# Performance work log

Hardware: AMD Instinct MI355X
Metric: run time of the kernel (lower is better)

## Reference

```python
import jax, jax.numpy as jnp
import numpy as np

EDGE_TEXT_IMG = 2
D_MODEL = 256
N_HEADS = 8
N_LAYERS = 3
INPUT_DIM = 768
LN_EPS = 1e-5
CONFLICT_EPS = 1e-6


def setup_inputs() -> dict:
    key = jax.random.key(0)
    ks = jax.random.split(key, 32)
    B, N, E = 16, 512, 4096
    d, H, L = D_MODEL, N_HEADS, N_LAYERS
    s = 0.02
    inp = {
        'node_feats': jax.random.normal(ks[0], (B, N, INPUT_DIM), jnp.float32),
        'node_mask': jnp.ones((B, N), bool),
        'text_mask': jax.random.randint(ks[1], (B, N), 0, 2).astype(bool),
        'image_mask': jax.random.randint(ks[2], (B, N), 0, 2).astype(bool),
        'global_indices': jax.random.randint(ks[3], (B,), 0, N),
        'edge_index': jax.random.randint(ks[4], (B, 2, E), 0, N),
        'edge_type': jax.random.randint(ks[5], (B, E), 0, 4),
        'edge_weight': jax.random.uniform(ks[6], (B, E), jnp.float32),
        # params
        'W_in': jax.random.normal(ks[7], (INPUT_DIM, d)) * s,
        'b_in': jnp.zeros((d,)),
        'Wqkv': jax.random.normal(ks[8], (L, d, 3 * d)) * s,
        'bqkv': jnp.zeros((L, 3 * d)),
        'Wo': jax.random.normal(ks[9], (L, d, d)) * s,
        'bo': jnp.zeros((L, d)),
        'ln1_g': jnp.ones((L, d)), 'ln1_b': jnp.zeros((L, d)),
        'ln2_g': jnp.ones((L, d)), 'ln2_b': jnp.zeros((L, d)),
        'Wff1': jax.random.normal(ks[10], (L, d, 4 * d)) * s,
        'bff1': jnp.zeros((L, 4 * d)),
        'Wff2': jax.random.normal(ks[11], (L, 4 * d, d)) * s,
        'bff2': jnp.zeros((L, d)),
        'et_emb': jax.random.normal(ks[12], (4, H)) * s,
        'Wm1': jax.random.normal(ks[13], (3 * d + 1, 2 * d)) * s,
        'bm1': jnp.zeros((2 * d,)),
        'Wm2': jax.random.normal(ks[14], (2 * d, d)) * s,
        'bm2': jnp.zeros((d,)),
        'Wm3': jax.random.normal(ks[15], (d, 1)) * s,
        'bm3': jnp.zeros((1,)),
    }
    return inp


def _ln(x, g, b):
    mu = jnp.mean(x, -1, keepdims=True)
    var = jnp.mean((x - mu) ** 2, -1, keepdims=True)
    return (x - mu) * jax.lax.rsqrt(var + LN_EPS) * g + b


def _build_bias(edge_index, edge_type, edge_weight, et_emb, N):
    # vectorized scatter-add of per-edge head biases into dense [B,H,N,N]
    B = edge_index.shape[0]
    src, dst = edge_index[:, 0], edge_index[:, 1]  # [B,E]
    vals = et_emb[edge_type]  # [B,E,H]
    vals = vals + jnp.where(edge_type == EDGE_TEXT_IMG, edge_weight, 0.0)[..., None]
    bias = jnp.zeros((B, N, N, et_emb.shape[1]), vals.dtype)
    bias = bias.at[jnp.arange(B)[:, None], src, dst].add(vals)
    return bias.transpose(0, 3, 1, 2)  # [B,H,N,N]


def _forward(node_feats, node_mask, text_mask, image_mask, global_indices,
             edge_index, edge_type, edge_weight,
             W_in, b_in, Wqkv, bqkv, Wo, bo, ln1_g, ln1_b, ln2_g, ln2_b,
             Wff1, bff1, Wff2, bff2, et_emb, Wm1, bm1, Wm2, bm2, Wm3, bm3):
    B, N, _ = node_feats.shape
    H = N_HEADS
    hd = D_MODEL // H
    attn_bias = _build_bias(edge_index, edge_type, edge_weight, et_emb, N)
    x = node_feats @ W_in + b_in  # [B,N,d]
    key_mask = node_mask[:, None, None, :]  # [B,1,1,N]
    for l in range(N_LAYERS):
        qkv = x @ Wqkv[l] + bqkv[l]
        qkv = qkv.reshape(B, N, 3, H, hd).transpose(2, 0, 3, 1, 4)
        q, k, v = qkv[0], qkv[1], qkv[2]  # [B,H,N,hd]
        scores = jnp.einsum('bhnd,bhmd->bhnm', q, k) / np.sqrt(hd).astype(np.float32)
        scores = scores + attn_bias
        scores = jnp.where(key_mask, scores, -jnp.inf)
        attn = jax.nn.softmax(scores, axis=-1)
        out = jnp.einsum('bhnm,bhmd->bhnd', attn, v)
        out = out.transpose(0, 2, 1, 3).reshape(B, N, D_MODEL)
        out = out @ Wo[l] + bo[l]
        x = _ln(x + out, ln1_g[l], ln1_b[l])
        ff = jax.nn.gelu(x @ Wff1[l] + bff1[l], approximate=False) @ Wff2[l] + bff2[l]
        x = _ln(x + ff, ln2_g[l], ln2_b[l])
    tm = text_mask.astype(x.dtype)
    im = image_mask.astype(x.dtype)
    tc = jnp.clip(tm.sum(1, keepdims=True), 1.0)
    ic = jnp.clip(im.sum(1, keepdims=True), 1.0)
    text_pool = (x * tm[..., None]).sum(1) / tc
    image_pool = (x * im[..., None]).sum(1) / ic
    global_embeds = x[jnp.arange(B), global_indices]
    n1 = jnp.maximum(jnp.linalg.norm(text_pool, axis=-1), CONFLICT_EPS)
    n2 = jnp.maximum(jnp.linalg.norm(image_pool, axis=-1), CONFLICT_EPS)
    cos = jnp.sum(text_pool * image_pool, -1) / (n1 * n2)
    conflict = (1.0 - cos)[:, None]
    combined = jnp.concatenate([global_embeds, text_pool, image_pool, conflict], -1)
    h = jax.nn.gelu(combined @ Wm1 + bm1, approximate=False)
    h = jax.nn.gelu(h @ Wm2 + bm2, approximate=False)
    logits = (h @ Wm3 + bm3)[:, 0]
    return logits


def reference(node_feats, node_mask, text_mask, image_mask, global_indices,
              edge_index, edge_type, edge_weight,
              W_in, b_in, Wqkv, bqkv, Wo, bo, ln1_g, ln1_b, ln2_g, ln2_b,
              Wff1, bff1, Wff2, bff2, et_emb, Wm1, bm1, Wm2, bm2, Wm3, bm3):
    return _forward(node_feats, node_mask, text_mask, image_mask, global_indices,
                    edge_index, edge_type, edge_weight,
                    W_in, b_in, Wqkv, bqkv, Wo, bo, ln1_g, ln1_b, ln2_g, ln2_b,
                    Wff1, bff1, Wff2, bff2, et_emb, Wm1, bm1, Wm2, bm2, Wm3, bm3)
```

## Files before the change

### kernel.cpp

```cpp
#include <hip/hip_runtime.h>
#include <hip/hip_bf16.h>
#include <math.h>

#define Bb 16
#define Nn 512
#define Dd 256
#define Hh 8
#define HD 32
#define Ll 3
#define INDIM 768
#define Ee 4096
#define FF 1024
#define KP3 36
#define KP2 72
#define NBUCK 32768

typedef unsigned short u16;
typedef __bf16 bf16x8 __attribute__((ext_vector_type(8)));
typedef float f32x4 __attribute__((ext_vector_type(4)));
typedef u16 us8 __attribute__((ext_vector_type(8)));
typedef u16 us4 __attribute__((ext_vector_type(4)));

__device__ __forceinline__ float gelu_exact(float x) {
    return 0.5f * x * (1.0f + erff(x * 0.70710678118654752f));
}

__device__ __forceinline__ u16 f2bf(float x) {
    union { __bf16 b; u16 u; } cv;
    cv.b = (__bf16)x;
    return cv.u;
}
__device__ __forceinline__ float bf2f(u16 h) {
    return __uint_as_float(((unsigned int)h) << 16);
}

__device__ __forceinline__ int ebucket(int b, int src, int dst) {
    return ((b * 32 + (src >> 4)) * 4 + (dst >> 7)) * 16 + (src & 15);
}

__device__ __forceinline__ int xcd_swz(int bid, int nwg) {
    int chunk = nwg >> 3;
    return (bid & 7) * chunk + (bid >> 3);
}


__global__ __launch_bounds__(256) void zero2_kernel(int* __restrict__ a, int na,
                                                    int* __restrict__ b, int nb) {
    int gid = blockIdx.x * 256 + threadIdx.x;
    if (gid < na) a[gid] = 0;
    else {
        int j = gid - na;
        if (j < nb) b[j] = 0;
    }
}

__global__ __launch_bounds__(256) void count_kernel(const int* __restrict__ edge_index,
                                                    int* __restrict__ counts) {
    int gid = blockIdx.x * 256 + threadIdx.x;
    int b = gid >> 12;
    int e = gid & (Ee - 1);
    int src = edge_index[b * 2 * Ee + e];
    int dst = edge_index[b * 2 * Ee + Ee + e];
    atomicAdd(&counts[ebucket(b, src, dst)], 1);
}

__global__ __launch_bounds__(1024) void scan_kernel(const int* __restrict__ counts,
                                                    int* __restrict__ offsets,
                                                    int* __restrict__ cursor) {
    __shared__ int ssum[1024];
    int t = threadIdx.x;
    int local[32];
    int s = 0;
#pragma unroll
    for (int i = 0; i < 32; i++) { local[i] = counts[t * 32 + i]; s += local[i]; }
    ssum[t] = s;
    __syncthreads();
    for (int off = 1; off < 1024; off *= 2) {
        __syncthreads();
        int v = (t >= off) ? ssum[t - off] : 0;
        __syncthreads();
        ssum[t] += v;
    }
    __syncthreads();
    int base = (t > 0) ? ssum[t - 1] : 0;
#pragma unroll
    for (int i = 0; i < 32; i++) {
        offsets[t * 32 + i] = base;
        cursor[t * 32 + i] = base;
        base += local[i];
    }
    if (t == 1023) offsets[NBUCK] = base;
}

__global__ __launch_bounds__(256) void scatter_kernel(const int* __restrict__ edge_index,
                                                      const int* __restrict__ edge_type,
                                                      const float* __restrict__ edge_weight,
                                                      int* __restrict__ cursor,
                                                      int2* __restrict__ pelist) {
    int gid = blockIdx.x * 256 + threadIdx.x;
    int b = gid >> 12;
    int e = gid & (Ee - 1);
    int src = edge_index[b * 2 * Ee + e];
    int dst = edge_index[b * 2 * Ee + Ee + e];
    int ty = edge_type[b * Ee + e];
    float wgt = edge_weight[b * Ee + e];
    int pos = atomicAdd(&cursor[ebucket(b, src, dst)], 1);
    int2 pe;
    pe.x = (src << 20) | (dst << 4) | ty;
    pe.y = __float_as_int(wgt);
    pelist[pos] = pe;
}


#define OFF_IN  0
#define OFF_QKV 196608
#define OFF_O   786432
#define OFF_F1  983040
#define OFF_F2  1769472
#define W_TOTAL 2555904

__global__ __launch_bounds__(256) void wsplit_all(const float* __restrict__ W_in,
                                                  const float* __restrict__ Wqkv,
                                                  const float* __restrict__ Wo,
                                                  const float* __restrict__ Wff1,
                                                  const float* __restrict__ Wff2,
                                                  u16* __restrict__ wh,
                                                  u16* __restrict__ wl) {
    int bid = blockIdx.x;
    const float* W;
    u16 *Wh, *Wl;
    int K, N, nb, kb;
    if (bid < 96) {
        W = W_in; Wh = wh + OFF_IN; Wl = wl + OFF_IN;
        K = 768; N = 256; nb = 0; kb = bid;
    } else if (bid < 384) {
        int lb = bid - 96; int l = lb / 96; lb -= l * 96;
        W = Wqkv + (size_t)l * 196608;
        Wh = wh + OFF_QKV + (size_t)l * 196608;
        Wl = wl + OFF_QKV + (size_t)l * 196608;
        K = 256; N = 768; nb = lb % 3; kb = lb / 3;
    } else if (bid < 480) {
        int lb = bid - 384; int l = lb / 32; lb -= l * 32;
        W = Wo + (size_t)l * 65536;
        Wh = wh + OFF_O + (size_t)l * 65536;
        Wl = wl + OFF_O + (size_t)l * 65536;
        K = 256; N = 256; nb = 0; kb = lb;
    } else if (bid < 864) {
        int lb = bid - 480; int l = lb / 128; lb -= l * 128;
        W = Wff1 + (size_t)l * 262144;
        Wh = wh + OFF_F1 + (size_t)l * 262144;
        Wl = wl + OFF_F1 + (size_t)l * 262144;
        K = 256; N = 1024; nb = lb % 4; kb = lb / 4;
    } else {
        int lb = bid - 864; int l = lb / 128; lb -= l * 128;
        W = Wff2 + (size_t)l * 262144;
        Wh = wh + OFF_F2 + (size_t)l * 262144;
        Wl = wl + OFF_F2 + (size_t)l * 262144;
        K = 1024; N = 256; nb = 0; kb = lb;
    }
    int n = nb * 256 + threadIdx.x;
    int k0 = kb * 8;
    float w[8];
#pragma unroll
    for (int i = 0; i < 8; i++) w[i] = W[(size_t)(k0 + i) * N + n];
    u16 h[8], l[8];
#pragma unroll
    for (int i = 0; i < 8; i++) {
        h[i] = f2bf(w[i]);
        l[i] = f2bf(w[i] - bf2f(h[i]));
    }
    us8 hv = {h[0], h[1], h[2], h[3], h[4], h[5], h[6], h[7]};
    us8 lv = {l[0], l[1], l[2], l[3], l[4], l[5], l[6], l[7]};
    *(us8*)&Wh[(size_t)n * K + k0] = hv;
    *(us8*)&Wl[(size_t)n * K + k0] = lv;
}


__global__ __launch_bounds__(256, 2) void gemm_mfma64(const float* __restrict__ A,
                                                      const u16* __restrict__ Bh,
                                                      const u16* __restrict__ Bl,
                                                      const float* __restrict__ bias,
                                                      float* __restrict__ C,
                                                      int M, int K, int N, int act) {
    __shared__ u16 sAh[2][64 * KP2];
    __shared__ u16 sAl[2][64 * KP2];
    __shared__ u16 sBh[2][64 * KP2];
    __shared__ u16 sBl[2][64 * KP2];

    int t = threadIdx.x;
    int w = t >> 6, L = t & 63;
    int wr = w >> 1, wc = w & 1;
    int lane15 = L & 15, quad = L >> 4;
    int nbx = N >> 6;
    int orig = xcd_swz(blockIdx.x, gridDim.x);
    int by = orig / nbx;
    int bx = orig - by * nbx;
    int row0 = by * 64, col0 = bx * 64;

    f32x4 acc[2][2];
#pragma unroll
    for (int mi = 0; mi < 2; mi++)
#pragma unroll
        for (int ni = 0; ni < 2; ni++) acc[mi][ni] = {0.f, 0.f, 0.f, 0.f};

    int ar0 = t >> 3, ak0 = (t & 7) * 8;
    int bn0 = t >> 2, bk0 = (t & 3) * 16;

    const float* Ap0 = &A[(size_t)(row0 + ar0) * K + ak0];
    const float* Ap1 = &A[(size_t)(row0 + ar0 + 32) * K + ak0];
    const u16* Bhp = &Bh[(size_t)(col0 + bn0) * K + bk0];
    const u16* Blp = &Bl[(size_t)(col0 + bn0) * K + bk0];

    float4 av0[2], av1[2];
    us8 bhv[2], blv[2];
#pragma unroll
    for (int j = 0; j < 2; j++) {
        av0[j] = *(const float4*)&Ap0[4 * j];
        av1[j] = *(const float4*)&Ap1[4 * j];
        bhv[j] = *(const us8*)&Bhp[8 * j];
        blv[j] = *(const us8*)&Blp[8 * j];
    }

    int nit = K >> 6;

#pragma unroll
    for (int j = 0; j < 2; j++) {
        {
            float a[4] = {av0[j].x, av0[j].y, av0[j].z, av0[j].w};
            u16 h[4], l[4];
#pragma unroll
            for (int q = 0; q < 4; q++) { h[q] = f2bf(a[q]); l[q] = f2bf(a[q] - bf2f(h[q])); }
            us4 hv = {h[0], h[1], h[2], h[3]};
            us4 lv = {l[0], l[1], l[2], l[3]};
            *(us4*)&sAh[0][ar0 * KP2 + ak0 + 4 * j] = hv;
            *(us4*)&sAl[0][ar0 * KP2 + ak0 + 4 * j] = lv;
        }
        {
            float a[4] = {av1[j].x, av1[j].y, av1[j].z, av1[j].w};
            u16 h[4], l[4];
#pragma unroll
            for (int q = 0; q < 4; q++) { h[q] = f2bf(a[q]); l[q] = f2bf(a[q] - bf2f(h[q])); }
            us4 hv = {h[0], h[1], h[2], h[3]};
            us4 lv = {l[0], l[1], l[2], l[3]};
            *(us4*)&sAh[0][(ar0 + 32) * KP2 + ak0 + 4 * j] = hv;
            *(us4*)&sAl[0][(ar0 + 32) * KP2 + ak0 + 4 * j] = lv;
        }
        *(us8*)&sBh[0][bn0 * KP2 + bk0 + 8 * j] = bhv[j];
        *(us8*)&sBl[0][bn0 * KP2 + bk0 + 8 * j] = blv[j];
    }
    if (nit > 1) {
#pragma unroll
        for (int j = 0; j < 2; j++) {
            av0[j] = *(const float4*)&Ap0[64 + 4 * j];
            av1[j] = *(const float4*)&Ap1[64 + 4 * j];
            bhv[j] = *(const us8*)&Bhp[64 + 8 * j];
            blv[j] = *(const us8*)&Blp[64 + 8 * j];
        }
    }

    for (int i = 0; i < nit; i++) {
        __syncthreads();
        int cur = i & 1;
        if (i + 1 < nit) {
            int nxt = cur ^ 1;
#pragma unroll
            for (int j = 0; j < 2; j++) {
                {
                    float a[4] = {av0[j].x, av0[j].y, av0[j].z, av0[j].w};
                    u16 h[4], l[4];
#pragma unroll
                    for (int q = 0; q < 4; q++) { h[q] = f2bf(a[q]); l[q] = f2bf(a[q] - bf2f(h[q])); }
                    us4 hv = {h[0], h[1], h[2], h[3]};
                    us4 lv = {l[0], l[1], l[2], l[3]};
                    *(us4*)&sAh[nxt][ar0 * KP2 + ak0 + 4 * j] = hv;
                    *(us4*)&sAl[nxt][ar0 * KP2 + ak0 + 4 * j] = lv;
                }
                {
                    float a[4] = {av1[j].x, av1[j].y, av1[j].z, av1[j].w};
                    u16 h[4], l[4];
#pragma unroll
                    for (int q = 0; q < 4; q++) { h[q] = f2bf(a[q]); l[q] = f2bf(a[q] - bf2f(h[q])); }
                    us4 hv = {h[0], h[1], h[2], h[3]};
                    us4 lv = {l[0], l[1], l[2], l[3]};
                    *(us4*)&sAh[nxt][(ar0 + 32) * KP2 + ak0 + 4 * j] = hv;
                    *(us4*)&sAl[nxt][(ar0 + 32) * KP2 + ak0 + 4 * j] = lv;
                }
                *(us8*)&sBh[nxt][bn0 * KP2 + bk0 + 8 * j] = bhv[j];
                *(us8*)&sBl[nxt][bn0 * KP2 + bk0 + 8 * j] = blv[j];
            }
            if (i + 2 < nit) {
                int ko = (i + 2) * 64;
#pragma unroll
                for (int j = 0; j < 2; j++) {
                    av0[j] = *(const float4*)&Ap0[ko + 4 * j];
                    av1[j] = *(const float4*)&Ap1[ko + 4 * j];
                    bhv[j] = *(const us8*)&Bhp[ko + 8 * j];
                    blv[j] = *(const us8*)&Blp[ko + 8 * j];
                }
            }
        }

#pragma unroll
        for (int half = 0; half < 2; half++) {
            int kof = half * 32 + quad * 8;
            us8 ahr[2], alr[2], bhr[2], blr[2];
#pragma unroll
            for (int mi = 0; mi < 2; mi++) {
                int ro = (wr * 32 + mi * 16 + lane15) * KP2 + kof;
                ahr[mi] = *(const us8*)&sAh[cur][ro];
                alr[mi] = *(const us8*)&sAl[cur][ro];
            }
#pragma unroll
            for (int ni = 0; ni < 2; ni++) {
                int ro = (wc * 32 + ni * 16 + lane15) * KP2 + kof;
                bhr[ni] = *(const us8*)&sBh[cur][ro];
                blr[ni] = *(const us8*)&sBl[cur][ro];
            }
#pragma unroll
            for (int mi = 0; mi < 2; mi++) {
                bf16x8 ah = *(const bf16x8*)&ahr[mi];
                bf16x8 al = *(const bf16x8*)&alr[mi];
#pragma unroll
                for (int ni = 0; ni < 2; ni++) {
                    bf16x8 bh = *(const bf16x8*)&bhr[ni];
                    bf16x8 bl = *(const bf16x8*)&blr[ni];
                    acc[mi][ni] = __builtin_amdgcn_mfma_f32_16x16x32_bf16(ah, bh, acc[mi][ni], 0, 0, 0);
                    acc[mi][ni] = __builtin_amdgcn_mfma_f32_16x16x32_bf16(ah, bl, acc[mi][ni], 0, 0, 0);
                    acc[mi][ni] = __builtin_amdgcn_mfma_f32_16x16x32_bf16(al, bh, acc[mi][ni], 0, 0, 0);
                }
            }
        }
    }

#pragma unroll
    for (int mi = 0; mi < 2; mi++) {
#pragma unroll
        for (int ni = 0; ni < 2; ni++) {
            int col = col0 + wc * 32 + ni * 16 + lane15;
            float bcol = bias[col];
#pragma unroll
            for (int r = 0; r < 4; r++) {
                int row = row0 + wr * 32 + mi * 16 + quad * 4 + r;
                float u = acc[mi][ni][r] + bcol;
                if (act == 1) u = gelu_exact(u);
                C[(size_t)row * N + col] = u;
            }
        }
    }
}


__global__ __launch_bounds__(512, 2) void gemm_mfma128(const float* __restrict__ A,
                                                       const u16* __restrict__ Bh,
                                                       const u16* __restrict__ Bl,
                                                       const float* __restrict__ bias,
                                                       float* __restrict__ C,
                                                       int M, int K, int N, int act) {
    __shared__ u16 sAh[2][128 * KP3];
    __shared__ u16 sAl[2][128 * KP3];
    __shared__ u16 sBh[2][128 * KP3];
    __shared__ u16 sBl[2][128 * KP3];

    int t = threadIdx.x;
    int w = t >> 6, L = t & 63;
    int wr = w >> 2, wc = w & 3;
    int lane15 = L & 15, quad = L >> 4;
    int nbx = N >> 7;
    int orig = xcd_swz(blockIdx.x, gridDim.x);
    int by = orig / nbx;
    int bx = orig - by * nbx;
    int row0 = by * 128, col0 = bx * 128;

    f32x4 acc[4][2];
#pragma unroll
    for (int mi = 0; mi < 4; mi++)
#pragma unroll
        for (int ni = 0; ni < 2; ni++) acc[mi][ni] = {0.f, 0.f, 0.f, 0.f};

    int ar0 = t >> 2, ak0 = (t & 3) * 8;
    int bn0 = t >> 2, bk0 = (t & 3) * 8;

    const float* Ap = &A[(size_t)(row0 + ar0) * K + ak0];
    const u16* Bhp = &Bh[(size_t)(col0 + bn0) * K + bk0];
    const u16* Blp = &Bl[(size_t)(col0 + bn0) * K + bk0];

    float4 av[2];
    us8 bhv, blv;
    av[0] = *(const float4*)&Ap[0];
    av[1] = *(const float4*)&Ap[4];
    bhv = *(const us8*)&Bhp[0];
    blv = *(const us8*)&Blp[0];

    int nit = K >> 5;

    {
        float a[8] = {av[0].x, av[0].y, av[0].z, av[0].w, av[1].x, av[1].y, av[1].z, av[1].w};
        u16 h[8], l[8];
#pragma unroll
        for (int q = 0; q < 8; q++) { h[q] = f2bf(a[q]); l[q] = f2bf(a[q] - bf2f(h[q])); }
        us8 hv = {h[0], h[1], h[2], h[3], h[4], h[5], h[6], h[7]};
        us8 lv = {l[0], l[1], l[2], l[3], l[4], l[5], l[6], l[7]};
        *(us8*)&sAh[0][ar0 * KP3 + ak0] = hv;
        *(us8*)&sAl[0][ar0 * KP3 + ak0] = lv;
        *(us8*)&sBh[0][bn0 * KP3 + bk0] = bhv;
        *(us8*)&sBl[0][bn0 * KP3 + bk0] = blv;
    }
    if (nit > 1) {
        av[0] = *(const float4*)&Ap[32];
        av[1] = *(const float4*)&Ap[36];
        bhv = *(const us8*)&Bhp[32];
        blv = *(const us8*)&Blp[32];
    }

    for (int it = 0; it < nit; it++) {
        __syncthreads();
        int cur = it & 1;
        if (it + 1 < nit) {
            int nxt = cur ^ 1;
            float a[8] = {av[0].x, av[0].y, av[0].z, av[0].w, av[1].x, av[1].y, av[1].z, av[1].w};
            u16 h[8], l[8];
#pragma unroll
            for (int q = 0; q < 8; q++) { h[q] = f2bf(a[q]); l[q] = f2bf(a[q] - bf2f(h[q])); }
            us8 hv = {h[0], h[1], h[2], h[3], h[4], h[5], h[6], h[7]};
            us8 lv = {l[0], l[1], l[2], l[3], l[4], l[5], l[6], l[7]};
            *(us8*)&sAh[nxt][ar0 * KP3 + ak0] = hv;
            *(us8*)&sAl[nxt][ar0 * KP3 + ak0] = lv;
            *(us8*)&sBh[nxt][bn0 * KP3 + bk0] = bhv;
            *(us8*)&sBl[nxt][bn0 * KP3 + bk0] = blv;
            if (it + 2 < nit) {
                int ko = (it + 2) * 32;
                av[0] = *(const float4*)&Ap[ko];
                av[1] = *(const float4*)&Ap[ko + 4];
                bhv = *(const us8*)&Bhp[ko];
                blv = *(const us8*)&Blp[ko];
            }
        }

        int kof = quad * 8;
        us8 ahr[4], alr[4], bhr[2], blr[2];
#pragma unroll
        for (int mi = 0; mi < 4; mi++) {
            int ro = (wr * 64 + mi * 16 + lane15) * KP3 + kof;
            ahr[mi] = *(const us8*)&sAh[cur][ro];
            alr[mi] = *(const us8*)&sAl[cur][ro];
        }
#pragma unroll
        for (int ni = 0; ni < 2; ni++) {
            int ro = (wc * 32 + ni * 16 + lane15) * KP3 + kof;
            bhr[ni] = *(const us8*)&sBh[cur][ro];
            blr[ni] = *(const us8*)&sBl[cur][ro];
        }
#pragma unroll
        for (int mi = 0; mi < 4; mi++) {
            bf16x8 ah = *(const bf16x8*)&ahr[mi];
            bf16x8 al = *(const bf16x8*)&alr[mi];
#pragma unroll
            for (int ni = 0; ni < 2; ni++) {
                bf16x8 bh = *(const bf16x8*)&bhr[ni];
                bf16x8 bl = *(const bf16x8*)&blr[ni];
                acc[mi][ni] = __builtin_amdgcn_mfma_f32_16x16x32_bf16(ah, bh, acc[mi][ni], 0, 0, 0);
                acc[mi][ni] = __builtin_amdgcn_mfma_f32_16x16x32_bf16(ah, bl, acc[mi][ni], 0, 0, 0);
                acc[mi][ni] = __builtin_amdgcn_mfma_f32_16x16x32_bf16(al, bh, acc[mi][ni], 0, 0, 0);
            }
        }
    }

#pragma unroll
    for (int mi = 0; mi < 4; mi++) {
#pragma unroll
        for (int ni = 0; ni < 2; ni++) {
            int col = col0 + wc * 32 + ni * 16 + lane15;
            float bcol = bias[col];
#pragma unroll
            for (int r = 0; r < 4; r++) {
                int row = row0 + wr * 64 + mi * 16 + quad * 4 + r;
                float u = acc[mi][ni][r] + bcol;
                if (act == 1) u = gelu_exact(u);
                C[(size_t)row * N + col] = u;
            }
        }
    }
}


#define SBP 132

__global__ __launch_bounds__(256, 2) void attn_kernel(const float* __restrict__ qkv,
                                                      const int* __restrict__ node_mask,
                                                      const int* __restrict__ offsets,
                                                      const int2* __restrict__ pelist,
                                                      const float* __restrict__ et_emb,
                                                      float* __restrict__ outbuf) {
    int bid = xcd_swz(blockIdx.x, gridDim.x);
    int quarter = bid & 3;
    int h = (bid >> 2) & 7;
    int b = bid >> 5;
    int t = threadIdx.x;
    int w = t >> 6, L = t & 63;
    int quad = L >> 4, lane15 = L & 15;
    int q8 = quad * 8;

    __shared__ u16 sKh[128 * 40];
    __shared__ u16 sKl[128 * 40];
    __shared__ u16 sVh[32 * SBP];
    __shared__ u16 sVl[32 * SBP];
    __shared__ float sS[4 * 16 * SBP];

    float* Sw = &sS[w * 16 * SBP];
    const float scale = 0.17677669529663687f;
    int nbase = quarter * 128 + w * 32;
    int mt0 = t >> 5, dt = t & 31;

    float etl0 = et_emb[0 * Hh + h];
    float etl1 = et_emb[1 * Hh + h];
    float etl2 = et_emb[2 * Hh + h];
    float etl3 = et_emb[3 * Hh + h];

    us8 Qh[2], Ql[2];
#pragma unroll
    for (int sub = 0; sub < 2; sub++) {
        size_t row = (size_t)(b * Nn + nbase + sub * 16 + lane15);
        float4 qa = *(const float4*)&qkv[row * 768 + h * HD + q8];
        float4 qb = *(const float4*)&qkv[row * 768 + h * HD + q8 + 4];
        float qv[8] = {qa.x, qa.y, qa.z, qa.w, qb.x, qb.y, qb.z, qb.w};
#pragma unroll
        for (int j = 0; j < 8; j++) {
            float xq = qv[j] * scale;
            u16 hh = f2bf(xq);
            Qh[sub][j] = hh;
            Ql[sub][j] = f2bf(xq - bf2f(hh));
        }
    }

    float Mst[2] = {-INFINITY, -INFINITY};
    float Lst[2] = {0.0f, 0.0f};
    f32x4 O[2][2];
#pragma unroll
    for (int sub = 0; sub < 2; sub++)
#pragma unroll
        for (int dc = 0; dc < 2; dc++) O[sub][dc] = {0.f, 0.f, 0.f, 0.f};

    float pk[16], pv[16];
#pragma unroll
    for (int j = 0; j < 16; j++) {
        size_t grow = (size_t)(b * Nn + mt0 + 8 * j) * 768 + h * HD + dt;
        pk[j] = qkv[grow + 256];
        pv[j] = qkv[grow + 512];
    }

    for (int T = 0; T < 4; T++) {
        int m0 = T * 128;
        __syncthreads();
#pragma unroll
        for (int j = 0; j < 16; j++) {
            int m = mt0 + 8 * j;
            u16 kh = f2bf(pk[j]);
            sKh[m * 40 + dt] = kh;
            sKl[m * 40 + dt] = f2bf(pk[j] - bf2f(kh));
            u16 vh = f2bf(pv[j]);
            sVh[dt * SBP + m] = vh;
            sVl[dt * SBP + m] = f2bf(pv[j] - bf2f(vh));
        }
        __syncthreads();
        if (T < 3) {
#pragma unroll
            for (int j = 0; j < 16; j++) {
                size_t grow = (size_t)(b * Nn + (T + 1) * 128 + mt0 + 8 * j) * 768 + h * HD + dt;
                pk[j] = qkv[grow + 256];
                pv[j] = qkv[grow + 512];
            }
        }

        float mk[4][8];
#pragma unroll
        for (int c = 0; c < 4; c++) {
            int4 u0 = *(const int4*)&node_mask[b * Nn + m0 + c * 32 + q8];
            int4 u1 = *(const int4*)&node_mask[b * Nn + m0 + c * 32 + q8 + 4];
            mk[c][0] = u0.x ? 0.f : -INFINITY;
            mk[c][1] = u0.y ? 0.f : -INFINITY;
            mk[c][2] = u0.z ? 0.f : -INFINITY;
            mk[c][3] = u0.w ? 0.f : -INFINITY;
            mk[c][4] = u1.x ? 0.f : -INFINITY;
            mk[c][5] = u1.y ? 0.f : -INFINITY;
            mk[c][6] = u1.z ? 0.f : -INFINITY;
            mk[c][7] = u1.w ? 0.f : -INFINITY;
        }

#pragma unroll
        for (int sub = 0; sub < 2; sub++) {
            int nsub = nbase + sub * 16;
            bf16x8 qh = *(const bf16x8*)&Qh[sub];
            bf16x8 ql = *(const bf16x8*)&Ql[sub];

            f32x4 accS[8];
#pragma unroll
            for (int mc = 0; mc < 8; mc++) accS[mc] = {0.f, 0.f, 0.f, 0.f};
#pragma unroll
            for (int mc = 0; mc < 8; mc++) {
                us8 khr = *(const us8*)&sKh[(mc * 16 + lane15) * 40 + q8];
                us8 klr = *(const us8*)&sKl[(mc * 16 + lane15) * 40 + q8];
                bf16x8 kh = *(const bf16x8*)&khr;
                bf16x8 kl = *(const bf16x8*)&klr;
                accS[mc] = __builtin_amdgcn_mfma_f32_16x16x32_bf16(qh, kh, accS[mc], 0, 0, 0);
                accS[mc] = __builtin_amdgcn_mfma_f32_16x16x32_bf16(qh, kl, accS[mc], 0, 0, 0);
                accS[mc] = __builtin_amdgcn_mfma_f32_16x16x32_bf16(ql, kh, accS[mc], 0, 0, 0);
            }
#pragma unroll
            for (int mc = 0; mc < 8; mc++)
#pragma unroll
                for (int r = 0; r < 4; r++)
                    Sw[(quad * 4 + r) * SBP + mc * 16 + lane15] = accS[mc][r];
            asm volatile("s_waitcnt lgkmcnt(0)" ::: "memory");

            int gb = ((b * 32 + (nsub >> 4)) * 4 + T) * 16;
            int beg = offsets[gb];
            int end = offsets[gb + 16];
            for (int i = beg + L; i < end; i += 64) {
                int2 pe = pelist[i];
                int sx = pe.x >> 20;
                int dx = (pe.x >> 4) & 511;
                int ty = pe.x & 3;
                float wgt = __int_as_float(pe.y);
                float val = (ty == 0) ? etl0 : (ty == 1) ? etl1 : (ty == 2) ? etl2 : etl3;
                if (ty == 2) val += wgt;
                atomicAdd(&Sw[(sx - nsub) * SBP + (dx - m0)], val);
            }
            asm volatile("s_waitcnt lgkmcnt(0)" ::: "memory");

            float s[4][8];
#pragma unroll
            for (int c = 0; c < 4; c++) {
                float4 a = *(const float4*)&Sw[lane15 * SBP + c * 32 + q8];
                float4 bq = *(const float4*)&Sw[lane15 * SBP + c * 32 + q8 + 4];
                s[c][0] = a.x + mk[c][0];  s[c][1] = a.y + mk[c][1];
                s[c][2] = a.z + mk[c][2];  s[c][3] = a.w + mk[c][3];
                s[c][4] = bq.x + mk[c][4]; s[c][5] = bq.y + mk[c][5];
                s[c][6] = bq.z + mk[c][6]; s[c][7] = bq.w + mk[c][7];
            }
            float mx = s[0][0];
#pragma unroll
            for (int c = 0; c < 4; c++)
#pragma unroll
                for (int j = 0; j < 8; j++) mx = fmaxf(mx, s[c][j]);
            mx = fmaxf(mx, __shfl_xor(mx, 16));
            mx = fmaxf(mx, __shfl_xor(mx, 32));
            float Mnew = fmaxf(Mst[sub], mx);
            float alpha = __expf(Mst[sub] - Mnew);
            float rs = 0.0f;
#pragma unroll
            for (int c = 0; c < 4; c++)
#pragma unroll
                for (int j = 0; j < 8; j++) {
                    s[c][j] = __expf(s[c][j] - Mnew);
                    rs += s[c][j];
                }
            rs += __shfl_xor(rs, 16);
            rs += __shfl_xor(rs, 32);
            Lst[sub] = Lst[sub] * alpha + rs;
            Mst[sub] = Mnew;

            us8 Ph[4], Pl[4];
#pragma unroll
            for (int c = 0; c < 4; c++)
#pragma unroll
                for (int j = 0; j < 8; j++) {
                    u16 ph = f2bf(s[c][j]);
                    Ph[c][j] = ph;
                    Pl[c][j] = f2bf(s[c][j] - bf2f(ph));
                }

            float aD[4];
#pragma unroll
            for (int r = 0; r < 4; r++) aD[r] = __shfl(alpha, (L & 48) | (quad * 4 + r));
#pragma unroll
            for (int dc = 0; dc < 2; dc++)
#pragma unroll
                for (int r = 0; r < 4; r++) O[sub][dc][r] *= aD[r];

#pragma unroll
            for (int c = 0; c < 4; c++) {
                bf16x8 ph = *(const bf16x8*)&Ph[c];
                bf16x8 pl = *(const bf16x8*)&Pl[c];
#pragma unroll
                for (int dc = 0; dc < 2; dc++) {
                    us8 vhr = *(const us8*)&sVh[(dc * 16 + lane15) * SBP + c * 32 + q8];
                    us8 vlr = *(const us8*)&sVl[(dc * 16 + lane15) * SBP + c * 32 + q8];
                    bf16x8 vh = *(const bf16x8*)&vhr;
                    bf16x8 vl = *(const bf16x8*)&vlr;
                    O[sub][dc] = __builtin_amdgcn_mfma_f32_16x16x32_bf16(ph, vh, O[sub][dc], 0, 0, 0);
                    O[sub][dc] = __builtin_amdgcn_mfma_f32_16x16x32_bf16(ph, vl, O[sub][dc], 0, 0, 0);
                    O[sub][dc] = __builtin_amdgcn_mfma_f32_16x16x32_bf16(pl, vh, O[sub][dc], 0, 0, 0);
                }
            }
        }
    }

#pragma unroll
    for (int sub = 0; sub < 2; sub++) {
        float linv = 1.0f / Lst[sub];
        float lD[4];
#pragma unroll
        for (int r = 0; r < 4; r++) lD[r] = __shfl(linv, (L & 48) | (quad * 4 + r));
#pragma unroll
        for (int dc = 0; dc < 2; dc++)
#pragma unroll
            for (int r = 0; r < 4; r++) {
                int row = nbase + sub * 16 + quad * 4 + r;
                outbuf[(size_t)(b * Nn + row) * Dd + h * HD + dc * 16 + lane15] =
                    O[sub][dc][r] * lD[r];
            }
    }
}


__global__ __launch_bounds__(256) void ln_kernel(float* __restrict__ x,
                                                 const float* __restrict__ res,
                                                 const float* __restrict__ g,
                                                 const float* __restrict__ bta) {
    int row = blockIdx.x * 4 + (threadIdx.x >> 6);
    int L = threadIdx.x & 63;
    size_t base = (size_t)row * Dd + L * 4;
    float4 v4 = *(const float4*)&x[base];
    float4 r4 = *(const float4*)&res[base];
    float v0 = v4.x + r4.x, v1 = v4.y + r4.y, v2 = v4.z + r4.z, v3 = v4.w + r4.w;
    float sm = v0 + v1 + v2 + v3;
#pragma unroll
    for (int o = 32; o > 0; o >>= 1) sm += __shfl_xor(sm, o);
    float mu = sm * (1.0f / Dd);
    float d0 = v0 - mu, d1 = v1 - mu, d2 = v2 - mu, d3 = v3 - mu;
    float s2 = d0 * d0 + d1 * d1 + d2 * d2 + d3 * d3;
#pragma unroll
    for (int o = 32; o > 0; o >>= 1) s2 += __shfl_xor(s2, o);
    float rsig = 1.0f / sqrtf(s2 * (1.0f / Dd) + 1e-5f);
    float4 g4 = *(const float4*)&g[L * 4];
    float4 b4 = *(const float4*)&bta[L * 4];
    float4 o4;
    o4.x = d0 * rsig * g4.x + b4.x;
    o4.y = d1 * rsig * g4.y + b4.y;
    o4.z = d2 * rsig * g4.z + b4.z;
    o4.w = d3 * rsig * g4.w + b4.w;
    *(float4*)&x[base] = o4;
}


__global__ __launch_bounds__(256) void pool_kernel(const float* __restrict__ x,
                                                   const int* __restrict__ text_mask,
                                                   const int* __restrict__ image_mask,
                                                   float* __restrict__ pools) {
    int b = blockIdx.y;
    int n0 = blockIdx.x * 32;
    int t = threadIdx.x;
    float tp = 0.0f, ip = 0.0f, c1 = 0.0f, c2 = 0.0f;
    for (int n = n0; n < n0 + 32; n++) {
        float xv = x[(size_t)(b * Nn + n) * Dd + t];
        int tm = text_mask[b * Nn + n];
        int im = image_mask[b * Nn + n];
        tp += tm ? xv : 0.0f;
        ip += im ? xv : 0.0f;
        c1 += (float)tm;
        c2 += (float)im;
    }
    atomicAdd(&pools[b * 514 + t], tp);
    atomicAdd(&pools[b * 514 + 256 + t], ip);
    if (t == 0) {
        atomicAdd(&pools[b * 514 + 512], c1);
        atomicAdd(&pools[b * 514 + 513], c2);
    }
}

__global__ __launch_bounds__(256) void comb_kernel(const float* __restrict__ x,
                                                   const float* __restrict__ pools,
                                                   const int* __restrict__ gidx,
                                                   float* __restrict__ comb) {
    int b = blockIdx.x;
    int t = threadIdx.x;
    __shared__ float redd[12];
    float tc = fmaxf(pools[b * 514 + 512], 1.0f);
    float ic = fmaxf(pools[b * 514 + 513], 1.0f);
    float tp = pools[b * 514 + t] / tc;
    float ip = pools[b * 514 + 256 + t] / ic;
    int gi = gidx[b];
    comb[b * 776 + t] = x[(size_t)(b * Nn + gi) * Dd + t];
    comb[b * 776 + 256 + t] = tp;
    comb[b * 776 + 512 + t] = ip;
    float dotv = tp * ip, n1v = tp * tp, n2v = ip * ip;
    for (int o = 32; o > 0; o >>= 1) {
        dotv += __shfl_down(dotv, o);
        n1v += __shfl_down(n1v, o);
        n2v += __shfl_down(n2v, o);
    }
    if ((t & 63) == 0) { redd[t >> 6] = dotv; redd[4 + (t >> 6)] = n1v; redd[8 + (t >> 6)] = n2v; }
    __syncthreads();
    if (t == 0) {
        float dd = redd[0] + redd[1] + redd[2] + redd[3];
        float a1 = fmaxf(sqrtf(redd[4] + redd[5] + redd[6] + redd[7]), 1e-6f);
        float a2 = fmaxf(sqrtf(redd[8] + redd[9] + redd[10] + redd[11]), 1e-6f);
        comb[b * 776 + 768] = 1.0f - dd / (a1 * a2);
    }
}

__global__ __launch_bounds__(256) void h1_kernel(const float* __restrict__ comb,
                                                 const float* __restrict__ Wm1,
                                                 const float* __restrict__ bm1,
                                                 float* __restrict__ h1) {
    int b = blockIdx.y;
    int jc = blockIdx.x;
    int t = threadIdx.x;
    __shared__ float scomb[776];
    __shared__ float partial[2][128];
    for (int i = t; i < 769; i += 256) scomb[i] = comb[b * 776 + i];
    __syncthreads();
    int j = jc * 128 + (t & 127);
    int kh = t >> 7;
    int kbeg = kh ? 384 : 0;
    int kend = kh ? 769 : 384;
    float acc = 0.0f;
#pragma unroll 8
    for (int k = kbeg; k < kend; k++) acc += scomb[k] * Wm1[k * 512 + j];
    partial[kh][t & 127] = acc;
    __syncthreads();
    if (t < 128) {
        float v = partial[0][t] + partial[1][t] + bm1[jc * 128 + t];
        h1[b * 512 + jc * 128 + t] = gelu_exact(v);
    }
}

__global__ __launch_bounds__(256) void head_fin(const float* __restrict__ h1,
                                                const float* __restrict__ Wm2,
                                                const float* __restrict__ bm2,
                                                const float* __restrict__ Wm3,
                                                const float* __restrict__ bm3,
                                                float* __restrict__ out) {
    int b = blockIdx.x;
    int t = threadIdx.x;
    __shared__ float h1s[512];
    __shared__ float red[4];
    for (int i = t; i < 512; i += 256) h1s[i] = h1[b * 512 + i];
    __syncthreads();
    float acc = bm2[t];
#pragma unroll 8
    for (int k = 0; k < 512; k++) acc += h1s[k] * Wm2[k * 256 + t];
    float h2 = gelu_exact(acc);
    float lv = h2 * Wm3[t];
    for (int o = 32; o > 0; o >>= 1) lv += __shfl_down(lv, o);
    if ((t & 63) == 0) red[t >> 6] = lv;
    __syncthreads();
    if (t == 0) out[b] = red[0] + red[1] + red[2] + red[3] + bm3[0];
}


extern "C" void kernel_launch(void* const* d_in, const int* in_sizes, int n_in,
                              void* d_out, int out_size, void* d_ws, size_t ws_size,
                              hipStream_t stream) {
    const float* node_feats = (const float*)d_in[0];
    const int* node_mask = (const int*)d_in[1];
    const int* text_mask = (const int*)d_in[2];
    const int* image_mask = (const int*)d_in[3];
    const int* gidx = (const int*)d_in[4];
    const int* edge_index = (const int*)d_in[5];
    const int* edge_type = (const int*)d_in[6];
    const float* edge_weight = (const float*)d_in[7];
    const float* W_in = (const float*)d_in[8];
    const float* b_in = (const float*)d_in[9];
    const float* Wqkv = (const float*)d_in[10];
    const float* bqkv = (const float*)d_in[11];
    const float* Wo = (const float*)d_in[12];
    const float* bo = (const float*)d_in[13];
    const float* ln1_g = (const float*)d_in[14];
    const float* ln1_b = (const float*)d_in[15];
    const float* ln2_g = (const float*)d_in[16];
    const float* ln2_b = (const float*)d_in[17];
    const float* Wff1 = (const float*)d_in[18];
    const float* bff1 = (const float*)d_in[19];
    const float* Wff2 = (const float*)d_in[20];
    const float* bff2 = (const float*)d_in[21];
    const float* et_emb = (const float*)d_in[22];
    const float* Wm1 = (const float*)d_in[23];
    const float* bm1 = (const float*)d_in[24];
    const float* Wm2 = (const float*)d_in[25];
    const float* bm2 = (const float*)d_in[26];
    const float* Wm3 = (const float*)d_in[27];
    const float* bm3 = (const float*)d_in[28];

    const int M = Bb * Nn;
    char* ws = (char*)d_ws;
    size_t off = 0;
    auto alloc = [&](size_t bytes) {
        void* p = ws + off;
        off += (bytes + 255) & ~(size_t)255;
        return p;
    };
    float* x = (float*)alloc((size_t)M * Dd * 4);
    float* qkvb = (float*)alloc((size_t)M * FF * 4);
    float* ffb = qkvb;
    float* attnout = (float*)alloc((size_t)M * Dd * 4);
    float* projb = (float*)alloc((size_t)M * Dd * 4);
    int* counts = (int*)alloc((size_t)NBUCK * 4);
    int* offsets = (int*)alloc((size_t)(NBUCK + 1) * 4);
    int* cursor = (int*)alloc((size_t)NBUCK * 4);
    int2* pelist = (int2*)alloc((size_t)Bb * Ee * 8);
    float* pools = (float*)alloc((size_t)Bb * 514 * 4);
    float* comb = (float*)alloc((size_t)Bb * 776 * 4);
    float* h1 = (float*)alloc((size_t)Bb * 512 * 4);
    u16* wh = (u16*)alloc((size_t)W_TOTAL * 2);
    u16* wl = (u16*)alloc((size_t)W_TOTAL * 2);
    (void)ws_size;

    zero2_kernel<<<(NBUCK + Bb * 514 + 255) / 256, 256, 0, stream>>>(
        counts, NBUCK, (int*)pools, Bb * 514);
    count_kernel<<<256, 256, 0, stream>>>(edge_index, counts);
    scan_kernel<<<1, 1024, 0, stream>>>(counts, offsets, cursor);
    scatter_kernel<<<256, 256, 0, stream>>>(edge_index, edge_type, edge_weight, cursor, pelist);

    wsplit_all<<<1248, 256, 0, stream>>>(W_in, Wqkv, Wo, Wff1, Wff2, wh, wl);

    gemm_mfma64<<<(Dd / 64) * (M / 64), 256, 0, stream>>>(
        node_feats, wh + OFF_IN, wl + OFF_IN, b_in, x, M, INDIM, Dd, 0);

    for (int l = 0; l < Ll; l++) {
        gemm_mfma128<<<(768 / 128) * (M / 128), 512, 0, stream>>>(
            x, wh + OFF_QKV + (size_t)l * 196608, wl + OFF_QKV + (size_t)l * 196608,
            bqkv + l * 768, qkvb, M, Dd, 768, 0);
        attn_kernel<<<Bb * Hh * 4, 256, 0, stream>>>(
            qkvb, node_mask, offsets, pelist, et_emb, attnout);
        gemm_mfma64<<<(Dd / 64) * (M / 64), 256, 0, stream>>>(
            attnout, wh + OFF_O + (size_t)l * 65536, wl + OFF_O + (size_t)l * 65536,
            bo + l * Dd, projb, M, Dd, Dd, 0);
        ln_kernel<<<M / 4, 256, 0, stream>>>(x, projb, ln1_g + l * Dd, ln1_b + l * Dd);
        gemm_mfma128<<<(FF / 128) * (M / 128), 512, 0, stream>>>(
            x, wh + OFF_F1 + (size_t)l * 262144, wl + OFF_F1 + (size_t)l * 262144,
            bff1 + l * FF, ffb, M, Dd, FF, 1);
        gemm_mfma64<<<(Dd / 64) * (M / 64), 256, 0, stream>>>(
            ffb, wh + OFF_F2 + (size_t)l * 262144, wl + OFF_F2 + (size_t)l * 262144,
            bff2 + l * Dd, projb, M, FF, Dd, 0);
        ln_kernel<<<M / 4, 256, 0, stream>>>(x, projb, ln2_g + l * Dd, ln2_b + l * Dd);
    }

    pool_kernel<<<dim3(16, Bb), 256, 0, stream>>>(x, text_mask, image_mask, pools);
    comb_kernel<<<Bb, 256, 0, stream>>>(x, pools, gidx, comb);
    h1_kernel<<<dim3(4, Bb), 256, 0, stream>>>(comb, Wm1, bm1, h1);
    head_fin<<<Bb, 256, 0, stream>>>(h1, Wm2, bm2, Wm3, bm3, (float*)d_out);
}
```

Measured before the change: 550.1 us.

## Single-buffer LDS in GEMM to raise occupancy to four blocks per CU

Replaces the double-buffered shared-memory pipeline in the split-bf16 MFMA GEMM with a single buffer and two barriers per K-step. The global prefetch for the next tile still runs in registers while the MFMA loop executes. This halves LDS use so launch bounds can ask for four blocks per CU instead of two, relying on more resident waves to hide latency. In exchange it adds a barrier per iteration and loses the overlap between LDS writes and compute within a block.

```diff
diff --git a/kernel.cpp b/kernel.cpp
--- a/kernel.cpp
+++ b/kernel.cpp
@@ -176,16 +176,16 @@
 }
 
 
-__global__ __launch_bounds__(256, 2) void gemm_mfma64(const float* __restrict__ A,
+__global__ __launch_bounds__(256, 4) void gemm_mfma64(const float* __restrict__ A,
                                                       const u16* __restrict__ Bh,
                                                       const u16* __restrict__ Bl,
                                                       const float* __restrict__ bias,
                                                       float* __restrict__ C,
                                                       int M, int K, int N, int act) {
-    __shared__ u16 sAh[2][64 * KP2];
-    __shared__ u16 sAl[2][64 * KP2];
-    __shared__ u16 sBh[2][64 * KP2];
-    __shared__ u16 sBl[2][64 * KP2];
+    __shared__ u16 sAh[64 * KP2];
+    __shared__ u16 sAl[64 * KP2];
+    __shared__ u16 sBh[64 * KP2];
+    __shared__ u16 sBl[64 * KP2];
 
     int t = threadIdx.x;
     int w = t >> 6, L = t & 63;
@@ -221,82 +221,42 @@
         blv[j] = *(const us8*)&Blp[8 * j];
     }
 
-    int nit = K >> 6;
-
-#pragma unroll
-    for (int j = 0; j < 2; j++) {
-        {
-            float a[4] = {av0[j].x, av0[j].y, av0[j].z, av0[j].w};
-            u16 h[4], l[4];
-#pragma unroll
-            for (int q = 0; q < 4; q++) { h[q] = f2bf(a[q]); l[q] = f2bf(a[q] - bf2f(h[q])); }
-            us4 hv = {h[0], h[1], h[2], h[3]};
-            us4 lv = {l[0], l[1], l[2], l[3]};
-            *(us4*)&sAh[0][ar0 * KP2 + ak0 + 4 * j] = hv;
-            *(us4*)&sAl[0][ar0 * KP2 + ak0 + 4 * j] = lv;
-        }
-        {
-            float a[4] = {av1[j].x, av1[j].y, av1[j].z, av1[j].w};
-            u16 h[4], l[4];
-#pragma unroll
-            for (int q = 0; q < 4; q++) { h[q] = f2bf(a[q]); l[q] = f2bf(a[q] - bf2f(h[q])); }
-            us4 hv = {h[0], h[1], h[2], h[3]};
-            us4 lv = {l[0], l[1], l[2], l[3]};
-            *(us4*)&sAh[0][(ar0 + 32) * KP2 + ak0 + 4 * j] = hv;
-            *(us4*)&sAl[0][(ar0 + 32) * KP2 + ak0 + 4 * j] = lv;
-        }
-        *(us8*)&sBh[0][bn0 * KP2 + bk0 + 8 * j] = bhv[j];
-        *(us8*)&sBl[0][bn0 * KP2 + bk0 + 8 * j] = blv[j];
-    }
-    if (nit > 1) {
+    for (int k0 = 0; k0 < K; k0 += 64) {
+        __syncthreads();
 #pragma unroll
         for (int j = 0; j < 2; j++) {
-            av0[j] = *(const float4*)&Ap0[64 + 4 * j];
-            av1[j] = *(const float4*)&Ap1[64 + 4 * j];
-            bhv[j] = *(const us8*)&Bhp[64 + 8 * j];
-            blv[j] = *(const us8*)&Blp[64 + 8 * j];
-        }
-    }
-
-    for (int i = 0; i < nit; i++) {
+            {
+                float a[4] = {av0[j].x, av0[j].y, av0[j].z, av0[j].w};
+                u16 h[4], l[4];
+#pragma unroll
+                for (int q = 0; q < 4; q++) { h[q] = f2bf(a[q]); l[q] = f2bf(a[q] - bf2f(h[q])); }
+                us4 hv = {h[0], h[1], h[2], h[3]};
+                us4 lv = {l[0], l[1], l[2], l[3]};
+                *(us4*)&sAh[ar0 * KP2 + ak0 + 4 * j] = hv;
+                *(us4*)&sAl[ar0 * KP2 + ak0 + 4 * j] = lv;
+            }
+            {
+                float a[4] = {av1[j].x, av1[j].y, av1[j].z, av1[j].w};
+                u16 h[4], l[4];
+#pragma unroll
+                for (int q = 0; q < 4; q++) { h[q] = f2bf(a[q]); l[q] = f2bf(a[q] - bf2f(h[q])); }
+                us4 hv = {h[0], h[1], h[2], h[3]};
+                us4 lv = {l[0], l[1], l[2], l[3]};
+                *(us4*)&sAh[(ar0 + 32) * KP2 + ak0 + 4 * j] = hv;
+                *(us4*)&sAl[(ar0 + 32) * KP2 + ak0 + 4 * j] = lv;
+            }
+            *(us8*)&sBh[bn0 * KP2 + bk0 + 8 * j] = bhv[j];
+            *(us8*)&sBl[bn0 * KP2 + bk0 + 8 * j] = blv[j];
+        }
         __syncthreads();
-        int cur = i & 1;
-        if (i + 1 < nit) {
-            int nxt = cur ^ 1;
+
+        if (k0 + 64 < K) {
 #pragma unroll
             for (int j = 0; j < 2; j++) {
-                {
-                    float a[4] = {av0[j].x, av0[j].y, av0[j].z, av0[j].w};
-                    u16 h[4], l[4];
-#pragma unroll
-                    for (int q = 0; q < 4; q++) { h[q] = f2bf(a[q]); l[q] = f2bf(a[q] - bf2f(h[q])); }
-                    us4 hv = {h[0], h[1], h[2], h[3]};
-                    us4 lv = {l[0], l[1], l[2], l[3]};
-                    *(us4*)&sAh[nxt][ar0 * KP2 + ak0 + 4 * j] = hv;
-                    *(us4*)&sAl[nxt][ar0 * KP2 + ak0 + 4 * j] = lv;
-                }
-                {
-                    float a[4] = {av1[j].x, av1[j].y, av1[j].z, av1[j].w};
-                    u16 h[4], l[4];
-#pragma unroll
-                    for (int q = 0; q < 4; q++) { h[q] = f2bf(a[q]); l[q] = f2bf(a[q] - bf2f(h[q])); }
-                    us4 hv = {h[0], h[1], h[2], h[3]};
-                    us4 lv = {l[0], l[1], l[2], l[3]};
-                    *(us4*)&sAh[nxt][(ar0 + 32) * KP2 + ak0 + 4 * j] = hv;
-                    *(us4*)&sAl[nxt][(ar0 + 32) * KP2 + ak0 + 4 * j] = lv;
-                }
-                *(us8*)&sBh[nxt][bn0 * KP2 + bk0 + 8 * j] = bhv[j];
-                *(us8*)&sBl[nxt][bn0 * KP2 + bk0 + 8 * j] = blv[j];
-            }
-            if (i + 2 < nit) {
-                int ko = (i + 2) * 64;
-#pragma unroll
-                for (int j = 0; j < 2; j++) {
-                    av0[j] = *(const float4*)&Ap0[ko + 4 * j];
-                    av1[j] = *(const float4*)&Ap1[ko + 4 * j];
-                    bhv[j] = *(const us8*)&Bhp[ko + 8 * j];
-                    blv[j] = *(const us8*)&Blp[ko + 8 * j];
-                }
+                av0[j] = *(const float4*)&Ap0[k0 + 64 + 4 * j];
+                av1[j] = *(const float4*)&Ap1[k0 + 64 + 4 * j];
+                bhv[j] = *(const us8*)&Bhp[k0 + 64 + 8 * j];
+                blv[j] = *(const us8*)&Blp[k0 + 64 + 8 * j];
             }
         }
 
@@ -307,14 +267,14 @@
 #pragma unroll
             for (int mi = 0; mi < 2; mi++) {
                 int ro = (wr * 32 + mi * 16 + lane15) * KP2 + kof;
-                ahr[mi] = *(const us8*)&sAh[cur][ro];
-                alr[mi] = *(const us8*)&sAl[cur][ro];
+                ahr[mi] = *(const us8*)&sAh[ro];
+                alr[mi] = *(const us8*)&sAl[ro];
             }
 #pragma unroll
             for (int ni = 0; ni < 2; ni++) {
                 int ro = (wc * 32 + ni * 16 + lane15) * KP2 + kof;
-                bhr[ni] = *(const us8*)&sBh[cur][ro];
-                blr[ni] = *(const us8*)&sBl[cur][ro];
+                bhr[ni] = *(const us8*)&sBh[ro];
+                blr[ni] = *(const us8*)&sBl[ro];
             }
 #pragma unroll
             for (int mi = 0; mi < 2; mi++) {
```

After: 561.7 us. 2.1% more time.
